# Kernel tuning notes

Hardware: AMD Instinct MI355X
Metric: run time of the kernel (lower is better)

The kernel has to match this reference:

```python
import jax, jax.numpy as jnp
import numpy as np

N = 50000
E = 800000
IN_C = 128
HID = 64
HEADS = 4
EPS = 1e-5
NEG_SLOPE = 0.2


def _glorot(key, shape, fan_in):
    return jax.random.normal(key, shape, dtype=jnp.float32) / np.sqrt(fan_in)


def setup_inputs() -> dict:
    key = jax.random.key(0)
    ks = jax.random.split(key, 32)
    d = {}
    d["x"] = jax.random.normal(ks[0], (N, IN_C), dtype=jnp.float32)
    d["edge_index"] = jax.random.randint(ks[1], (2, E), 0, N, dtype=jnp.int32)
    ph = HID // HEADS  # per-head channels for concat layers (16)
    # Layer 1: in -> [heads, ph], concat
    d["W1"] = _glorot(ks[2], (IN_C, HEADS * ph), IN_C)
    d["a1s"] = _glorot(ks[3], (HEADS, ph), ph)
    d["a1d"] = _glorot(ks[4], (HEADS, ph), ph)
    d["b1"] = jnp.zeros((HID,), jnp.float32)
    # Layer 2: hid -> [heads, ph], concat
    d["W2"] = _glorot(ks[5], (HID, HEADS * ph), HID)
    d["a2s"] = _glorot(ks[6], (HEADS, ph), ph)
    d["a2d"] = _glorot(ks[7], (HEADS, ph), ph)
    d["b2"] = jnp.zeros((HID,), jnp.float32)
    # Layer 3: hid -> [heads, HID], mean over heads (concat=False)
    d["W3"] = _glorot(ks[8], (HID, HEADS * HID), HID)
    d["a3s"] = _glorot(ks[9], (HEADS, HID), HID)
    d["a3d"] = _glorot(ks[10], (HEADS, HID), HID)
    d["b3"] = jnp.zeros((HID,), jnp.float32)
    # BatchNorms (eval mode: running stats)
    for i, k0 in zip((1, 2, 3), (11, 14, 17)):
        d[f"bn{i}_g"] = jnp.ones((HID,), jnp.float32)
        d[f"bn{i}_b"] = jnp.zeros((HID,), jnp.float32)
        d[f"bn{i}_m"] = 0.1 * jax.random.normal(ks[k0], (HID,), dtype=jnp.float32)
        d[f"bn{i}_v"] = jax.random.uniform(ks[k0 + 1], (HID,), minval=0.5, maxval=1.5, dtype=jnp.float32)
    # Classifier MLP: HID -> HID//2 -> 1
    d["cW1"] = _glorot(ks[20], (HID, HID // 2), HID)
    d["cb1"] = jnp.zeros((HID // 2,), jnp.float32)
    d["cW2"] = _glorot(ks[21], (HID // 2, 1), HID // 2)
    d["cb2"] = jnp.zeros((1,), jnp.float32)
    return d


def _gat_layer(x, src, dst, W, a_s, a_d, b, concat):
    n = x.shape[0]
    heads, outc = a_s.shape
    h = (x @ W).reshape(n, heads, outc)           # [N,H,C]
    al_s = jnp.einsum("nhc,hc->nh", h, a_s)       # [N,H]
    al_d = jnp.einsum("nhc,hc->nh", h, a_d)
    e = jax.nn.leaky_relu(al_s[src] + al_d[dst], NEG_SLOPE)  # [E,H]
    m = jax.ops.segment_max(e, dst, num_segments=n)
    ex = jnp.exp(e - m[dst])
    den = jax.ops.segment_sum(ex, dst, num_segments=n)
    alpha = ex / den[dst]                          # segment softmax over dst
    out = jax.ops.segment_sum(h[src] * alpha[..., None], dst, num_segments=n)  # [N,H,C]
    if concat:
        out = out.reshape(n, heads * outc)
    else:
        out = out.mean(axis=1)
    return out + b


def _bn(x, g, b, m, v):
    return g * (x - m) * jax.lax.rsqrt(v + EPS) + b


def reference(x, edge_index, W1, a1s, a1d, b1, W2, a2s, a2d, b2, W3, a3s, a3d, b3,
              bn1_g, bn1_b, bn1_m, bn1_v, bn2_g, bn2_b, bn2_m, bn2_v,
              bn3_g, bn3_b, bn3_m, bn3_v, cW1, cb1, cW2, cb2):
    n = x.shape[0]
    # PyG GATConv adds self-loops by default
    loop = jnp.arange(n, dtype=edge_index.dtype)
    src = jnp.concatenate([edge_index[0], loop])
    dst = jnp.concatenate([edge_index[1], loop])

    h = _gat_layer(x, src, dst, W1, a1s, a1d, b1, concat=True)
    h = jax.nn.elu(_bn(h, bn1_g, bn1_b, bn1_m, bn1_v))
    h = _gat_layer(h, src, dst, W2, a2s, a2d, b2, concat=True)
    h = jax.nn.elu(_bn(h, bn2_g, bn2_b, bn2_m, bn2_v))
    h = _gat_layer(h, src, dst, W3, a3s, a3d, b3, concat=False)
    h = _bn(h, bn3_g, bn3_b, bn3_m, bn3_v)

    h = jax.nn.elu(h @ cW1 + cb1)
    out = (h @ cW2 + cb2).squeeze(-1)  # [N]
    return out
```

## Files before the change

### kernel.cpp

```cpp
#include <hip/hip_runtime.h>

#define HH 4

__device__ __forceinline__ float lrelu(float v){ return v > 0.f ? v : 0.2f*v; }

template<int IC>
__global__ void gemm_gat(const float* __restrict__ X, const float* __restrict__ W,
                         const float* __restrict__ a_s, const float* __restrict__ a_d,
                         float* __restrict__ h, float* __restrict__ als, float* __restrict__ ald,
                         int N) {
    int t = threadIdx.x, lane = t & 63, wid = t >> 6;
    int n = blockIdx.x*4 + wid;
    bool valid = n < N;
    int nc = valid ? n : N-1;
    __shared__ float xs[4][IC];
    #pragma unroll
    for (int k = lane; k < IC; k += 64) xs[wid][k] = X[(size_t)nc*IC + k];
    float acc = 0.f;
    #pragma unroll 8
    for (int k = 0; k < IC; ++k) acc += xs[wid][k] * W[k*64 + lane];
    if (valid) h[(size_t)nc*64 + lane] = acc;
    int hh = lane >> 4, c = lane & 15;
    float ps = acc * a_s[hh*16 + c];
    float pd = acc * a_d[hh*16 + c];
    #pragma unroll
    for (int m = 1; m < 16; m <<= 1){ ps += __shfl_xor(ps, m); pd += __shfl_xor(pd, m); }
    if (valid && c == 0){ als[nc*HH + hh] = ps; ald[nc*HH + hh] = pd; }
}


__global__ void zero_i32(int* __restrict__ p, int n){
    int i = blockIdx.x*256 + threadIdx.x;
    if (i < n) p[i] = 0;
}

__global__ void count_deg(const int* __restrict__ ei, int* __restrict__ deg, int E){
    int e = blockIdx.x*256 + threadIdx.x;
    if (e < E) atomicAdd(&deg[ei[E + e]], 1);
}

__global__ void deg_bsum(const int* __restrict__ deg, int* __restrict__ bsum, int N){
    int t = threadIdx.x;
    int base = blockIdx.x*1024 + t*4;
    int s = 0;
    if (base + 3 < N){
        int4 v = *(const int4*)(deg + base);
        s = v.x + v.y + v.z + v.w;
    } else {
        for (int q = 0; q < 4; ++q) if (base + q < N) s += deg[base + q];
    }
    #pragma unroll
    for (int m = 1; m < 64; m <<= 1) s += __shfl_xor(s, m);
    __shared__ int ws[4];
    if ((t & 63) == 0) ws[t >> 6] = s;
    __syncthreads();
    if (t == 0) bsum[blockIdx.x] = ws[0] + ws[1] + ws[2] + ws[3];
}

__global__ void scan_write(const int* __restrict__ deg, const int* __restrict__ bsum,
                           int* __restrict__ row_off, int* __restrict__ cursor, int N, int E){
    int t = threadIdx.x, bid = blockIdx.x, lane = t & 63, w = t >> 6;
    int base = bid*1024 + t*4;
    int v0 = 0, v1 = 0, v2 = 0, v3 = 0;
    if (base + 3 < N){
        int4 v = *(const int4*)(deg + base);
        v0 = v.x; v1 = v.y; v2 = v.z; v3 = v.w;
    } else {
        if (base     < N) v0 = deg[base];
        if (base + 1 < N) v1 = deg[base + 1];
        if (base + 2 < N) v2 = deg[base + 2];
        if (base + 3 < N) v3 = deg[base + 3];
    }
    int s = v0 + v1 + v2 + v3;
    int x = s;
    #pragma unroll
    for (int d = 1; d < 64; d <<= 1){
        int y = __shfl_up(x, d);
        if (lane >= d) x += y;
    }
    __shared__ int wsum[4];
    __shared__ int boff_s;
    if (lane == 63) wsum[w] = x;
    if (t < 64){
        int o = 0;
        for (int i = t; i < bid; i += 64) o += bsum[i];
        #pragma unroll
        for (int m = 1; m < 64; m <<= 1) o += __shfl_xor(o, m);
        if (t == 0) boff_s = o;
    }
    __syncthreads();
    int woff = 0;
    for (int i = 0; i < w; ++i) woff += wsum[i];
    int o = boff_s + woff + (x - s);
    if (base     < N){ row_off[base]     = o; cursor[base]     = o; o += v0; }
    if (base + 1 < N){ row_off[base + 1] = o; cursor[base + 1] = o; o += v1; }
    if (base + 2 < N){ row_off[base + 2] = o; cursor[base + 2] = o; o += v2; }
    if (base + 3 < N){ row_off[base + 3] = o; cursor[base + 3] = o; o += v3; }
    if (t == 0 && bid == 0) row_off[N] = E;
}

__global__ void fill_csr(const int* __restrict__ ei, int* __restrict__ cursor,
                         int* __restrict__ ssrc, int E){
    int e = blockIdx.x*256 + threadIdx.x;
    if (e < E){
        int d = ei[E + e];
        int p = atomicAdd(&cursor[d], 1);
        ssrc[p] = ei[e];
    }
}

__global__ void prep_l3(const float* __restrict__ W3, const float* __restrict__ a3s,
                        const float* __restrict__ a3d, float* __restrict__ ws3,
                        float* __restrict__ wd3, float* __restrict__ W3p){
    int t = threadIdx.x;
    int hh = t >> 6, k = t & 63;
    float ss = 0.f, sd = 0.f;
    for (int c = 0; c < 64; ++c){
        float w = W3[k*256 + hh*64 + c];
        ss += w * a3s[hh*64 + c];
        sd += w * a3d[hh*64 + c];
        W3p[t*64 + c] = 0.25f * w;
    }
    ws3[t] = ss; wd3[t] = sd;
}

template<bool L3PREP>
__global__ void gat_agg16(const int* __restrict__ row_off, const int* __restrict__ ssrc,
                          const float* __restrict__ als, const float* __restrict__ ald,
                          const float* __restrict__ h, const float* __restrict__ b,
                          const float* __restrict__ g, const float* __restrict__ bb,
                          const float* __restrict__ bm, const float* __restrict__ bv,
                          float* __restrict__ out,
                          const float* __restrict__ ws3, const float* __restrict__ wd3,
                          float* __restrict__ als3, float* __restrict__ ald3, int N){
    int t = threadIdx.x, lane = t & 63, wid = t >> 6;
    int n = blockIdx.x*4 + wid;
    if (n >= N) return;
    __shared__ float wl[4][16][4];
    __shared__ int   sl[4][16];
    int j  = lane & 15;
    int hh = lane >> 4;
    int cb = lane & 15;
    int gq = lane >> 4;
    int hd = cb >> 2;
    float ad_w = ald[n*HH + hh];
    float v_hd = __expf(lrelu(als[n*HH + hd] + ald[n*HH + hd]));
    int beg = row_off[n], end = row_off[n+1];
    float4 acc = make_float4(0.f, 0.f, 0.f, 0.f);
    if (lane < 16){
        float4 hs = *(const float4*)(h + (size_t)n*64 + cb*4);
        acc.x = v_hd*hs.x; acc.y = v_hd*hs.y; acc.z = v_hd*hs.z; acc.w = v_hd*hs.w;
    }
    float denp = 0.f;
    for (int c16 = beg; c16 < end; c16 += 16){
        int e = c16 + j;
        int s = n; float ev = 0.f;
        if (e < end){ s = ssrc[e]; ev = __expf(lrelu(als[s*HH + hh] + ad_w)); }
        denp += ev;
        wl[wid][j][hh] = ev;
        if (hh == 0) sl[wid][j] = s;
        int cnt = min(16, end - c16);
        for (int qb = 0; qb < cnt; qb += 8){
            int eA = qb + gq, eB = qb + 4 + gq;
            int   sA = sl[wid][eA],     sB = sl[wid][eB];
            float wA = wl[wid][eA][hd], wB = wl[wid][eB][hd];
            float4 hA = *(const float4*)(h + (size_t)sA*64 + cb*4);
            float4 hB = *(const float4*)(h + (size_t)sB*64 + cb*4);
            acc.x += wA*hA.x; acc.y += wA*hA.y; acc.z += wA*hA.z; acc.w += wA*hA.w;
            acc.x += wB*hB.x; acc.y += wB*hB.y; acc.z += wB*hB.z; acc.w += wB*hB.w;
        }
    }
    #pragma unroll
    for (int m = 1; m < 16; m <<= 1) denp += __shfl_xor(denp, m);
    float den = __shfl(denp, hd << 4) + v_hd;
    #pragma unroll
    for (int m = 16; m < 64; m <<= 1){
        acc.x += __shfl_xor(acc.x, m); acc.y += __shfl_xor(acc.y, m);
        acc.z += __shfl_xor(acc.z, m); acc.w += __shfl_xor(acc.w, m);
    }
    float4 bb4 = *(const float4*)(b  + cb*4);
    float4 gg4 = *(const float4*)(g  + cb*4);
    float4 be4 = *(const float4*)(bb + cb*4);
    float4 bm4 = *(const float4*)(bm + cb*4);
    float4 bv4 = *(const float4*)(bv + cb*4);
    float4 val;
    val.x = gg4.x*(acc.x/den + bb4.x - bm4.x)*rsqrtf(bv4.x + 1e-5f) + be4.x;
    val.y = gg4.y*(acc.y/den + bb4.y - bm4.y)*rsqrtf(bv4.y + 1e-5f) + be4.y;
    val.z = gg4.z*(acc.z/den + bb4.z - bm4.z)*rsqrtf(bv4.z + 1e-5f) + be4.z;
    val.w = gg4.w*(acc.w/den + bb4.w - bm4.w)*rsqrtf(bv4.w + 1e-5f) + be4.w;
    val.x = val.x > 0.f ? val.x : expm1f(val.x);
    val.y = val.y > 0.f ? val.y : expm1f(val.y);
    val.z = val.z > 0.f ? val.z : expm1f(val.z);
    val.w = val.w > 0.f ? val.w : expm1f(val.w);
    if (lane < 16) *(float4*)(out + (size_t)n*64 + cb*4) = val;
    if (L3PREP){
        float4 w_s = *(const float4*)(ws3 + gq*64 + cb*4);
        float4 w_d = *(const float4*)(wd3 + gq*64 + cb*4);
        float ps = val.x*w_s.x + val.y*w_s.y + val.z*w_s.z + val.w*w_s.w;
        float pd = val.x*w_d.x + val.y*w_d.y + val.z*w_d.z + val.w*w_d.w;
        #pragma unroll
        for (int m = 1; m < 16; m <<= 1){ ps += __shfl_xor(ps, m); pd += __shfl_xor(pd, m); }
        if (cb == 0){ als3[n*HH + gq] = ps; ald3[n*HH + gq] = pd; }
    }
}

__global__ void gat_agg3_fused(const int* __restrict__ row_off, const int* __restrict__ ssrc,
                               const float* __restrict__ als, const float* __restrict__ ald,
                               const float* __restrict__ hin, const float* __restrict__ W3p,
                               const float* __restrict__ b, const float* __restrict__ g,
                               const float* __restrict__ bb, const float* __restrict__ bm,
                               const float* __restrict__ bv, float* __restrict__ out, int N){
    int t = threadIdx.x, lane = t & 63, wid = t >> 6;
    int n0 = blockIdx.x*4;
    int n = min(n0 + wid, N-1);
    __shared__ __align__(16) float4 wlds[4][64];
    __shared__ int slds[4][64];
    __shared__ __align__(16) float ysh[4*256];
    __shared__ float red[4][4][64];
    int cb = lane & 15, gq = lane >> 4;
    float4 adv = *(const float4*)(ald + n*4);
    float4 av  = *(const float4*)(als + n*4);
    float v0 = __expf(lrelu(av.x + adv.x)), v1 = __expf(lrelu(av.y + adv.y));
    float v2 = __expf(lrelu(av.z + adv.z)), v3 = __expf(lrelu(av.w + adv.w));
    int beg = row_off[n], end = row_off[n+1];
    float4 acc0 = make_float4(0,0,0,0), acc1 = acc0, acc2 = acc0, acc3 = acc0;
    if (lane < 16){
        float4 hs = *(const float4*)(hin + (size_t)n*64 + cb*4);
        acc0.x = v0*hs.x; acc0.y = v0*hs.y; acc0.z = v0*hs.z; acc0.w = v0*hs.w;
        acc1.x = v1*hs.x; acc1.y = v1*hs.y; acc1.z = v1*hs.z; acc1.w = v1*hs.w;
        acc2.x = v2*hs.x; acc2.y = v2*hs.y; acc2.z = v2*hs.z; acc2.w = v2*hs.w;
        acc3.x = v3*hs.x; acc3.y = v3*hs.y; acc3.z = v3*hs.z; acc3.w = v3*hs.w;
    }
    float dp0 = 0.f, dp1 = 0.f, dp2 = 0.f, dp3 = 0.f;
    for (int c64 = beg; c64 < end; c64 += 64){
        int e = c64 + lane;
        int s = n; float e0 = 0.f, e1 = 0.f, e2 = 0.f, e3 = 0.f;
        if (e < end){
            s = ssrc[e];
            float4 a = *(const float4*)(als + s*4);
            e0 = __expf(lrelu(a.x + adv.x));
            e1 = __expf(lrelu(a.y + adv.y));
            e2 = __expf(lrelu(a.z + adv.z));
            e3 = __expf(lrelu(a.w + adv.w));
        }
        dp0 += e0; dp1 += e1; dp2 += e2; dp3 += e3;
        wlds[wid][lane] = make_float4(e0, e1, e2, e3);
        slds[wid][lane] = s;
        int cn = min(64, end - c64);
        for (int qb = 0; qb < cn; qb += 8){
            int eA = qb + gq, eB = qb + 4 + gq;
            int sA = slds[wid][eA], sB = slds[wid][eB];
            float4 wA = wlds[wid][eA], wB = wlds[wid][eB];
            float4 hA = *(const float4*)(hin + (size_t)sA*64 + cb*4);
            float4 hB = *(const float4*)(hin + (size_t)sB*64 + cb*4);
            acc0.x += wA.x*hA.x; acc0.y += wA.x*hA.y; acc0.z += wA.x*hA.z; acc0.w += wA.x*hA.w;
            acc1.x += wA.y*hA.x; acc1.y += wA.y*hA.y; acc1.z += wA.y*hA.z; acc1.w += wA.y*hA.w;
            acc2.x += wA.z*hA.x; acc2.y += wA.z*hA.y; acc2.z += wA.z*hA.z; acc2.w += wA.z*hA.w;
            acc3.x += wA.w*hA.x; acc3.y += wA.w*hA.y; acc3.z += wA.w*hA.z; acc3.w += wA.w*hA.w;
            acc0.x += wB.x*hB.x; acc0.y += wB.x*hB.y; acc0.z += wB.x*hB.z; acc0.w += wB.x*hB.w;
            acc1.x += wB.y*hB.x; acc1.y += wB.y*hB.y; acc1.z += wB.y*hB.z; acc1.w += wB.y*hB.w;
            acc2.x += wB.z*hB.x; acc2.y += wB.z*hB.y; acc2.z += wB.z*hB.z; acc2.w += wB.z*hB.w;
            acc3.x += wB.w*hB.x; acc3.y += wB.w*hB.y; acc3.z += wB.w*hB.z; acc3.w += wB.w*hB.w;
        }
    }
    #pragma unroll
    for (int m = 1; m < 64; m <<= 1){
        dp0 += __shfl_xor(dp0, m); dp1 += __shfl_xor(dp1, m);
        dp2 += __shfl_xor(dp2, m); dp3 += __shfl_xor(dp3, m);
    }
    #pragma unroll
    for (int m = 16; m < 64; m <<= 1){
        acc0.x += __shfl_xor(acc0.x, m); acc0.y += __shfl_xor(acc0.y, m);
        acc0.z += __shfl_xor(acc0.z, m); acc0.w += __shfl_xor(acc0.w, m);
        acc1.x += __shfl_xor(acc1.x, m); acc1.y += __shfl_xor(acc1.y, m);
        acc1.z += __shfl_xor(acc1.z, m); acc1.w += __shfl_xor(acc1.w, m);
        acc2.x += __shfl_xor(acc2.x, m); acc2.y += __shfl_xor(acc2.y, m);
        acc2.z += __shfl_xor(acc2.z, m); acc2.w += __shfl_xor(acc2.w, m);
        acc3.x += __shfl_xor(acc3.x, m); acc3.y += __shfl_xor(acc3.y, m);
        acc3.z += __shfl_xor(acc3.z, m); acc3.w += __shfl_xor(acc3.w, m);
    }
    if (lane < 16){
        float r0 = 1.f/(v0 + dp0), r1 = 1.f/(v1 + dp1);
        float r2 = 1.f/(v2 + dp2), r3 = 1.f/(v3 + dp3);
        float4 y0 = make_float4(acc0.x*r0, acc0.y*r0, acc0.z*r0, acc0.w*r0);
        float4 y1 = make_float4(acc1.x*r1, acc1.y*r1, acc1.z*r1, acc1.w*r1);
        float4 y2 = make_float4(acc2.x*r2, acc2.y*r2, acc2.z*r2, acc2.w*r2);
        float4 y3 = make_float4(acc3.x*r3, acc3.y*r3, acc3.z*r3, acc3.w*r3);
        *(float4*)&ysh[wid*256 +   0 + cb*4] = y0;
        *(float4*)&ysh[wid*256 +  64 + cb*4] = y1;
        *(float4*)&ysh[wid*256 + 128 + cb*4] = y2;
        *(float4*)&ysh[wid*256 + 192 + cb*4] = y3;
    }
    __syncthreads();
    float a0 = 0.f, a1 = 0.f, a2 = 0.f, a3 = 0.f;
    int jbase = wid*64;
    #pragma unroll 4
    for (int jj = 0; jj < 64; jj += 4){
        int jb = jbase + jj;
        float4 y0 = *(const float4*)&ysh[0*256 + jb];
        float4 y1 = *(const float4*)&ysh[1*256 + jb];
        float4 y2 = *(const float4*)&ysh[2*256 + jb];
        float4 y3 = *(const float4*)&ysh[3*256 + jb];
        float w0 = W3p[(jb    )*64 + lane];
        float w1 = W3p[(jb + 1)*64 + lane];
        float w2 = W3p[(jb + 2)*64 + lane];
        float w3 = W3p[(jb + 3)*64 + lane];
        a0 += y0.x*w0 + y0.y*w1 + y0.z*w2 + y0.w*w3;
        a1 += y1.x*w0 + y1.y*w1 + y1.z*w2 + y1.w*w3;
        a2 += y2.x*w0 + y2.y*w1 + y2.z*w2 + y2.w*w3;
        a3 += y3.x*w0 + y3.y*w1 + y3.z*w2 + y3.w*w3;
    }
    red[wid][0][lane] = a0;
    red[wid][1][lane] = a1;
    red[wid][2][lane] = a2;
    red[wid][3][lane] = a3;
    __syncthreads();
    int nw = n0 + wid;
    if (nw < N){
        float val = red[0][wid][lane] + red[1][wid][lane] +
                    red[2][wid][lane] + red[3][wid][lane] + b[lane];
        out[(size_t)nw*64 + lane] = g[lane]*(val - bm[lane])*rsqrtf(bv[lane] + 1e-5f) + bb[lane];
    }
}

__global__ void classifier(const float* __restrict__ hin, const float* __restrict__ cW1,
                           const float* __restrict__ cb1, const float* __restrict__ cW2,
                           const float* __restrict__ cb2, float* __restrict__ out, int N){
    __shared__ float w1[64*32];
    __shared__ float b1s[32], w2[32];
    int t = threadIdx.x;
    for (int k = t; k < 64*32; k += 256) w1[k] = cW1[k];
    if (t < 32) { b1s[t] = cb1[t]; w2[t] = cW2[t]; }
    __syncthreads();
    int n = blockIdx.x*256 + t;
    if (n >= N) return;
    float hrow[64];
    #pragma unroll
    for (int k = 0; k < 64; ++k) hrow[k] = hin[(size_t)n*64 + k];
    float acc2 = cb2[0];
    #pragma unroll 4
    for (int j = 0; j < 32; ++j) {
        float a = b1s[j];
        #pragma unroll
        for (int k = 0; k < 64; ++k) a += hrow[k]*w1[k*32 + j];
        float e = a > 0.f ? a : expm1f(a);
        acc2 += e * w2[j];
    }
    out[n] = acc2;
}

extern "C" void kernel_launch(void* const* d_in, const int* in_sizes, int n_in,
                              void* d_out, int out_size, void* d_ws, size_t ws_size,
                              hipStream_t stream) {
    const float* x    = (const float*)d_in[0];
    const int*   ei   = (const int*)  d_in[1];
    const float* W1   = (const float*)d_in[2];
    const float* a1s  = (const float*)d_in[3];
    const float* a1d  = (const float*)d_in[4];
    const float* b1   = (const float*)d_in[5];
    const float* W2   = (const float*)d_in[6];
    const float* a2s  = (const float*)d_in[7];
    const float* a2d  = (const float*)d_in[8];
    const float* b2   = (const float*)d_in[9];
    const float* W3   = (const float*)d_in[10];
    const float* a3s  = (const float*)d_in[11];
    const float* a3d  = (const float*)d_in[12];
    const float* b3   = (const float*)d_in[13];
    const float* bn1g = (const float*)d_in[14];
    const float* bn1b = (const float*)d_in[15];
    const float* bn1m = (const float*)d_in[16];
    const float* bn1v = (const float*)d_in[17];
    const float* bn2g = (const float*)d_in[18];
    const float* bn2b = (const float*)d_in[19];
    const float* bn2m = (const float*)d_in[20];
    const float* bn2v = (const float*)d_in[21];
    const float* bn3g = (const float*)d_in[22];
    const float* bn3b = (const float*)d_in[23];
    const float* bn3m = (const float*)d_in[24];
    const float* bn3v = (const float*)d_in[25];
    const float* cW1  = (const float*)d_in[26];
    const float* cb1  = (const float*)d_in[27];
    const float* cW2  = (const float*)d_in[28];
    const float* cb2  = (const float*)d_in[29];

    const int N = in_sizes[0] / 128;
    const int E = in_sizes[1] / 2;

    float* h    = (float*)d_ws;
    float* hin  = h    + (size_t)N*64;
    float* als  = hin  + (size_t)N*64;
    float* ald  = als  + (size_t)N*4;
    float* als3 = ald  + (size_t)N*4;
    float* ald3 = als3 + (size_t)N*4;
    float* ws3  = ald3 + (size_t)N*4;
    float* wd3  = ws3  + 256;
    float* W3p  = wd3  + 256;
    int* deg     = (int*)(W3p + 16384);
    int* row_off = deg + N;
    int* cursor  = row_off + (N + 1);
    int* ssrc    = cursor + N;
    int* bsum    = ssrc + E;

    const int B = 256;
    int gN  = (N + B-1)/B;
    int gE  = (E + B-1)/B;
    int NB  = (N + 1023)/1024;
    int gN4 = (N + 3)/4;

    zero_i32<<<gN, B, 0, stream>>>(deg, N);
    count_deg<<<gE, B, 0, stream>>>(ei, deg, E);
    deg_bsum<<<NB, B, 0, stream>>>(deg, bsum, N);
    scan_write<<<NB, B, 0, stream>>>(deg, bsum, row_off, cursor, N, E);
    fill_csr<<<gE, B, 0, stream>>>(ei, cursor, ssrc, E);
    prep_l3<<<1, 256, 0, stream>>>(W3, a3s, a3d, ws3, wd3, W3p);

    gemm_gat<128><<<gN4, B, 0, stream>>>(x, W1, a1s, a1d, h, als, ald, N);
    gat_agg16<false><<<gN4, B, 0, stream>>>(row_off, ssrc, als, ald, h, b1,
                                            bn1g, bn1b, bn1m, bn1v, hin,
                                            nullptr, nullptr, nullptr, nullptr, N);

    gemm_gat<64><<<gN4, B, 0, stream>>>(hin, W2, a2s, a2d, h, als, ald, N);
    gat_agg16<true><<<gN4, B, 0, stream>>>(row_off, ssrc, als, ald, h, b2,
                                           bn2g, bn2b, bn2m, bn2v, hin,
                                           ws3, wd3, als3, ald3, N);

    gat_agg3_fused<<<gN4, B, 0, stream>>>(row_off, ssrc, als3, ald3, hin, W3p,
                                          b3, bn3g, bn3b, bn3m, bn3v, h, N);

    classifier<<<gN, B, 0, stream>>>(h, cW1, cb1, cW2, cb2, (float*)d_out, N);
}
```

Baseline: 386.5 us.

## Fuse layer-2 GEMM into layer-1 aggregation and classifier into layer-3 kernel

The layer-1 aggregation kernel now also does the 64x64 layer-2 projection per node and computes its attention logits, so the separate gemm_gat<64> launch is gone. The classifier MLP moves into the end of the layer-3 aggregation kernel, using classifier weights staged in shared memory. This removes two launches and two full node-feature round trips through global memory. The gather loops are also widened to issue four neighbour loads per iteration. The costs are extra shared memory, higher register pressure in the fused kernels and a second node-feature buffer in the workspace.

```diff
diff --git a/kernel.cpp b/kernel.cpp
--- a/kernel.cpp
+++ b/kernel.cpp
@@ -124,15 +124,96 @@
     ws3[t] = ss; wd3[t] = sd;
 }
 
-template<bool L3PREP>
-__global__ void gat_agg16(const int* __restrict__ row_off, const int* __restrict__ ssrc,
-                          const float* __restrict__ als, const float* __restrict__ ald,
-                          const float* __restrict__ h, const float* __restrict__ b,
-                          const float* __restrict__ g, const float* __restrict__ bb,
-                          const float* __restrict__ bm, const float* __restrict__ bv,
-                          float* __restrict__ out,
-                          const float* __restrict__ ws3, const float* __restrict__ wd3,
-                          float* __restrict__ als3, float* __restrict__ ald3, int N){
+__global__ void gat_agg16_l1(const int* __restrict__ row_off, const int* __restrict__ ssrc,
+                             const float* __restrict__ als, const float* __restrict__ ald,
+                             const float* __restrict__ h, const float* __restrict__ b,
+                             const float* __restrict__ g, const float* __restrict__ bb,
+                             const float* __restrict__ bm, const float* __restrict__ bv,
+                             const float* __restrict__ W2, const float* __restrict__ a2s,
+                             const float* __restrict__ a2d, float* __restrict__ h2,
+                             float* __restrict__ als2, float* __restrict__ ald2, int N){
+    int t = threadIdx.x, lane = t & 63, wid = t >> 6;
+    __shared__ float wl[4][16][4];
+    __shared__ int   sl[4][16];
+    __shared__ __align__(16) float vb[4][64];
+    int n = blockIdx.x*4 + wid;
+    if (n >= N) return;
+    int j  = lane & 15;
+    int hh = lane >> 4;
+    int cb = lane & 15;
+    int gq = lane >> 4;
+    int hd = cb >> 2;
+    float ad_w = ald[n*HH + hh];
+    float v_hd = __expf(lrelu(als[n*HH + hd] + ald[n*HH + hd]));
+    int beg = row_off[n], end = row_off[n+1];
+    float4 acc = make_float4(0.f, 0.f, 0.f, 0.f);
+    if (lane < 16){
+        float4 hs = *(const float4*)(h + (size_t)n*64 + cb*4);
+        acc.x = v_hd*hs.x; acc.y = v_hd*hs.y; acc.z = v_hd*hs.z; acc.w = v_hd*hs.w;
+    }
+    float denp = 0.f;
+    for (int c16 = beg; c16 < end; c16 += 16){
+        int e = c16 + j;
+        int s = n; float ev = 0.f;
+        if (e < end){ s = ssrc[e]; ev = __expf(lrelu(als[s*HH + hh] + ad_w)); }
+        denp += ev;
+        wl[wid][j][hh] = ev;
+        if (hh == 0) sl[wid][j] = s;
+        int   s0 = sl[wid][gq],     s1 = sl[wid][4+gq];
+        int   s2 = sl[wid][8+gq],   s3 = sl[wid][12+gq];
+        float w0 = wl[wid][gq][hd], w1 = wl[wid][4+gq][hd];
+        float w2 = wl[wid][8+gq][hd], w3 = wl[wid][12+gq][hd];
+        float4 h0 = *(const float4*)(h + (size_t)s0*64 + cb*4);
+        float4 h1 = *(const float4*)(h + (size_t)s1*64 + cb*4);
+        float4 h2v = *(const float4*)(h + (size_t)s2*64 + cb*4);
+        float4 h3 = *(const float4*)(h + (size_t)s3*64 + cb*4);
+        acc.x += w0*h0.x + w1*h1.x + w2*h2v.x + w3*h3.x;
+        acc.y += w0*h0.y + w1*h1.y + w2*h2v.y + w3*h3.y;
+        acc.z += w0*h0.z + w1*h1.z + w2*h2v.z + w3*h3.z;
+        acc.w += w0*h0.w + w1*h1.w + w2*h2v.w + w3*h3.w;
+    }
+    #pragma unroll
+    for (int m = 1; m < 16; m <<= 1) denp += __shfl_xor(denp, m);
+    float den = __shfl(denp, hd << 4) + v_hd;
+    #pragma unroll
+    for (int m = 16; m < 64; m <<= 1){
+        acc.x += __shfl_xor(acc.x, m); acc.y += __shfl_xor(acc.y, m);
+        acc.z += __shfl_xor(acc.z, m); acc.w += __shfl_xor(acc.w, m);
+    }
+    float4 bb4 = *(const float4*)(b  + cb*4);
+    float4 gg4 = *(const float4*)(g  + cb*4);
+    float4 be4 = *(const float4*)(bb + cb*4);
+    float4 bm4 = *(const float4*)(bm + cb*4);
+    float4 bv4 = *(const float4*)(bv + cb*4);
+    float4 val;
+    val.x = gg4.x*(acc.x/den + bb4.x - bm4.x)*rsqrtf(bv4.x + 1e-5f) + be4.x;
+    val.y = gg4.y*(acc.y/den + bb4.y - bm4.y)*rsqrtf(bv4.y + 1e-5f) + be4.y;
+    val.z = gg4.z*(acc.z/den + bb4.z - bm4.z)*rsqrtf(bv4.z + 1e-5f) + be4.z;
+    val.w = gg4.w*(acc.w/den + bb4.w - bm4.w)*rsqrtf(bv4.w + 1e-5f) + be4.w;
+    val.x = val.x > 0.f ? val.x : expm1f(val.x);
+    val.y = val.y > 0.f ? val.y : expm1f(val.y);
+    val.z = val.z > 0.f ? val.z : expm1f(val.z);
+    val.w = val.w > 0.f ? val.w : expm1f(val.w);
+    if (lane < 16) *(float4*)&vb[wid][cb*4] = val;
+    float acc2 = 0.f;
+    #pragma unroll 8
+    for (int k = 0; k < 64; ++k) acc2 += vb[wid][k] * W2[k*64 + lane];
+    h2[(size_t)n*64 + lane] = acc2;
+    float ps = acc2 * a2s[hh*16 + j];
+    float pd = acc2 * a2d[hh*16 + j];
+    #pragma unroll
+    for (int m = 1; m < 16; m <<= 1){ ps += __shfl_xor(ps, m); pd += __shfl_xor(pd, m); }
+    if (j == 0){ als2[n*HH + hh] = ps; ald2[n*HH + hh] = pd; }
+}
+
+__global__ void gat_agg16_l2(const int* __restrict__ row_off, const int* __restrict__ ssrc,
+                             const float* __restrict__ als, const float* __restrict__ ald,
+                             const float* __restrict__ h, const float* __restrict__ b,
+                             const float* __restrict__ g, const float* __restrict__ bb,
+                             const float* __restrict__ bm, const float* __restrict__ bv,
+                             float* __restrict__ out,
+                             const float* __restrict__ ws3, const float* __restrict__ wd3,
+                             float* __restrict__ als3, float* __restrict__ ald3, int N){
     int t = threadIdx.x, lane = t & 63, wid = t >> 6;
     int n = blockIdx.x*4 + wid;
     if (n >= N) return;
@@ -159,16 +240,18 @@
         denp += ev;
         wl[wid][j][hh] = ev;
         if (hh == 0) sl[wid][j] = s;
-        int cnt = min(16, end - c16);
-        for (int qb = 0; qb < cnt; qb += 8){
-            int eA = qb + gq, eB = qb + 4 + gq;
-            int   sA = sl[wid][eA],     sB = sl[wid][eB];
-            float wA = wl[wid][eA][hd], wB = wl[wid][eB][hd];
-            float4 hA = *(const float4*)(h + (size_t)sA*64 + cb*4);
-            float4 hB = *(const float4*)(h + (size_t)sB*64 + cb*4);
-            acc.x += wA*hA.x; acc.y += wA*hA.y; acc.z += wA*hA.z; acc.w += wA*hA.w;
-            acc.x += wB*hB.x; acc.y += wB*hB.y; acc.z += wB*hB.z; acc.w += wB*hB.w;
-        }
+        int   s0 = sl[wid][gq],     s1 = sl[wid][4+gq];
+        int   s2 = sl[wid][8+gq],   s3 = sl[wid][12+gq];
+        float w0 = wl[wid][gq][hd], w1 = wl[wid][4+gq][hd];
+        float w2 = wl[wid][8+gq][hd], w3 = wl[wid][12+gq][hd];
+        float4 h0 = *(const float4*)(h + (size_t)s0*64 + cb*4);
+        float4 h1 = *(const float4*)(h + (size_t)s1*64 + cb*4);
+        float4 h2v = *(const float4*)(h + (size_t)s2*64 + cb*4);
+        float4 h3 = *(const float4*)(h + (size_t)s3*64 + cb*4);
+        acc.x += w0*h0.x + w1*h1.x + w2*h2v.x + w3*h3.x;
+        acc.y += w0*h0.y + w1*h1.y + w2*h2v.y + w3*h3.y;
+        acc.z += w0*h0.z + w1*h1.z + w2*h2v.z + w3*h3.z;
+        acc.w += w0*h0.w + w1*h1.w + w2*h2v.w + w3*h3.w;
     }
     #pragma unroll
     for (int m = 1; m < 16; m <<= 1) denp += __shfl_xor(denp, m);
@@ -193,15 +276,13 @@
     val.z = val.z > 0.f ? val.z : expm1f(val.z);
     val.w = val.w > 0.f ? val.w : expm1f(val.w);
     if (lane < 16) *(float4*)(out + (size_t)n*64 + cb*4) = val;
-    if (L3PREP){
-        float4 w_s = *(const float4*)(ws3 + gq*64 + cb*4);
-        float4 w_d = *(const float4*)(wd3 + gq*64 + cb*4);
-        float ps = val.x*w_s.x + val.y*w_s.y + val.z*w_s.z + val.w*w_s.w;
-        float pd = val.x*w_d.x + val.y*w_d.y + val.z*w_d.z + val.w*w_d.w;
-        #pragma unroll
-        for (int m = 1; m < 16; m <<= 1){ ps += __shfl_xor(ps, m); pd += __shfl_xor(pd, m); }
-        if (cb == 0){ als3[n*HH + gq] = ps; ald3[n*HH + gq] = pd; }
-    }
+    float4 w_s = *(const float4*)(ws3 + gq*64 + cb*4);
+    float4 w_d = *(const float4*)(wd3 + gq*64 + cb*4);
+    float ps = val.x*w_s.x + val.y*w_s.y + val.z*w_s.z + val.w*w_s.w;
+    float pd = val.x*w_d.x + val.y*w_d.y + val.z*w_d.z + val.w*w_d.w;
+    #pragma unroll
+    for (int m = 1; m < 16; m <<= 1){ ps += __shfl_xor(ps, m); pd += __shfl_xor(pd, m); }
+    if (cb == 0){ als3[n*HH + gq] = ps; ald3[n*HH + gq] = pd; }
 }
 
 __global__ void gat_agg3_fused(const int* __restrict__ row_off, const int* __restrict__ ssrc,
@@ -209,14 +290,23 @@
                                const float* __restrict__ hin, const float* __restrict__ W3p,
                                const float* __restrict__ b, const float* __restrict__ g,
                                const float* __restrict__ bb, const float* __restrict__ bm,
-                               const float* __restrict__ bv, float* __restrict__ out, int N){
+                               const float* __restrict__ bv,
+                               const float* __restrict__ cW1, const float* __restrict__ cb1,
+                               const float* __restrict__ cW2, const float* __restrict__ cb2,
+                               float* __restrict__ dout, int N){
     int t = threadIdx.x, lane = t & 63, wid = t >> 6;
     int n0 = blockIdx.x*4;
     int n = min(n0 + wid, N-1);
+    bool valid = (n0 + wid) < N;
     __shared__ __align__(16) float4 wlds[4][64];
     __shared__ int slds[4][64];
     __shared__ __align__(16) float ysh[4*256];
     __shared__ float red[4][4][64];
+    __shared__ float cls1[64*32];
+    __shared__ float clb[32], clw2[32];
+    __shared__ float ysc[4][64];
+    for (int k = t; k < 2048; k += 256) cls1[k] = cW1[k];
+    if (t < 32){ clb[t] = cb1[t]; clw2[t] = cW2[t]; }
     int cb = lane & 15, gq = lane >> 4;
     float4 adv = *(const float4*)(ald + n*4);
     float4 av  = *(const float4*)(als + n*4);
@@ -247,20 +337,31 @@
         wlds[wid][lane] = make_float4(e0, e1, e2, e3);
         slds[wid][lane] = s;
         int cn = min(64, end - c64);
-        for (int qb = 0; qb < cn; qb += 8){
-            int eA = qb + gq, eB = qb + 4 + gq;
-            int sA = slds[wid][eA], sB = slds[wid][eB];
-            float4 wA = wlds[wid][eA], wB = wlds[wid][eB];
+        for (int qb = 0; qb < cn; qb += 16){
+            int sA = slds[wid][qb + gq],      sB = slds[wid][qb + 4 + gq];
+            int sC = slds[wid][qb + 8 + gq],  sD = slds[wid][qb + 12 + gq];
+            float4 wA = wlds[wid][qb + gq],     wB = wlds[wid][qb + 4 + gq];
+            float4 wC = wlds[wid][qb + 8 + gq], wD = wlds[wid][qb + 12 + gq];
             float4 hA = *(const float4*)(hin + (size_t)sA*64 + cb*4);
             float4 hB = *(const float4*)(hin + (size_t)sB*64 + cb*4);
-            acc0.x += wA.x*hA.x; acc0.y += wA.x*hA.y; acc0.z += wA.x*hA.z; acc0.w += wA.x*hA.w;
-            acc1.x += wA.y*hA.x; acc1.y += wA.y*hA.y; acc1.z += wA.y*hA.z; acc1.w += wA.y*hA.w;
-            acc2.x += wA.z*hA.x; acc2.y += wA.z*hA.y; acc2.z += wA.z*hA.z; acc2.w += wA.z*hA.w;
-            acc3.x += wA.w*hA.x; acc3.y += wA.w*hA.y; acc3.z += wA.w*hA.z; acc3.w += wA.w*hA.w;
-            acc0.x += wB.x*hB.x; acc0.y += wB.x*hB.y; acc0.z += wB.x*hB.z; acc0.w += wB.x*hB.w;
-            acc1.x += wB.y*hB.x; acc1.y += wB.y*hB.y; acc1.z += wB.y*hB.z; acc1.w += wB.y*hB.w;
-            acc2.x += wB.z*hB.x; acc2.y += wB.z*hB.y; acc2.z += wB.z*hB.z; acc2.w += wB.z*hB.w;
-            acc3.x += wB.w*hB.x; acc3.y += wB.w*hB.y; acc3.z += wB.w*hB.z; acc3.w += wB.w*hB.w;
+            float4 hC = *(const float4*)(hin + (size_t)sC*64 + cb*4);
+            float4 hD = *(const float4*)(hin + (size_t)sD*64 + cb*4);
+            acc0.x += wA.x*hA.x + wB.x*hB.x + wC.x*hC.x + wD.x*hD.x;
+            acc0.y += wA.x*hA.y + wB.x*hB.y + wC.x*hC.y + wD.x*hD.y;
+            acc0.z += wA.x*hA.z + wB.x*hB.z + wC.x*hC.z + wD.x*hD.z;
+            acc0.w += wA.x*hA.w + wB.x*hB.w + wC.x*hC.w + wD.x*hD.w;
+            acc1.x += wA.y*hA.x + wB.y*hB.x + wC.y*hC.x + wD.y*hD.x;
+            acc1.y += wA.y*hA.y + wB.y*hB.y + wC.y*hC.y + wD.y*hD.y;
+            acc1.z += wA.y*hA.z + wB.y*hB.z + wC.y*hC.z + wD.y*hD.z;
+            acc1.w += wA.y*hA.w + wB.y*hB.w + wC.y*hC.w + wD.y*hD.w;
+            acc2.x += wA.z*hA.x + wB.z*hB.x + wC.z*hC.x + wD.z*hD.x;
+            acc2.y += wA.z*hA.y + wB.z*hB.y + wC.z*hC.y + wD.z*hD.y;
+            acc2.z += wA.z*hA.z + wB.z*hB.z + wC.z*hC.z + wD.z*hD.z;
+            acc2.w += wA.z*hA.w + wB.z*hB.w + wC.z*hC.w + wD.z*hD.w;
+            acc3.x += wA.w*hA.x + wB.w*hB.x + wC.w*hC.x + wD.w*hD.x;
+            acc3.y += wA.w*hA.y + wB.w*hB.y + wC.w*hC.y + wD.w*hD.y;
+            acc3.z += wA.w*hA.z + wB.w*hB.z + wC.w*hC.z + wD.w*hD.z;
+            acc3.w += wA.w*hA.w + wB.w*hB.w + wC.w*hC.w + wD.w*hD.w;
         }
     }
     #pragma unroll
@@ -282,14 +383,10 @@
     if (lane < 16){
         float r0 = 1.f/(v0 + dp0), r1 = 1.f/(v1 + dp1);
         float r2 = 1.f/(v2 + dp2), r3 = 1.f/(v3 + dp3);
-        float4 y0 = make_float4(acc0.x*r0, acc0.y*r0, acc0.z*r0, acc0.w*r0);
-        float4 y1 = make_float4(acc1.x*r1, acc1.y*r1, acc1.z*r1, acc1.w*r1);
-        float4 y2 = make_float4(acc2.x*r2, acc2.y*r2, acc2.z*r2, acc2.w*r2);
-        float4 y3 = make_float4(acc3.x*r3, acc3.y*r3, acc3.z*r3, acc3.w*r3);
-        *(float4*)&ysh[wid*256 +   0 + cb*4] = y0;
-        *(float4*)&ysh[wid*256 +  64 + cb*4] = y1;
-        *(float4*)&ysh[wid*256 + 128 + cb*4] = y2;
-        *(float4*)&ysh[wid*256 + 192 + cb*4] = y3;
+        *(float4*)&ysh[wid*256 +   0 + cb*4] = make_float4(acc0.x*r0, acc0.y*r0, acc0.z*r0, acc0.w*r0);
+        *(float4*)&ysh[wid*256 +  64 + cb*4] = make_float4(acc1.x*r1, acc1.y*r1, acc1.z*r1, acc1.w*r1);
+        *(float4*)&ysh[wid*256 + 128 + cb*4] = make_float4(acc2.x*r2, acc2.y*r2, acc2.z*r2, acc2.w*r2);
+        *(float4*)&ysh[wid*256 + 192 + cb*4] = make_float4(acc3.x*r3, acc3.y*r3, acc3.z*r3, acc3.w*r3);
     }
     __syncthreads();
     float a0 = 0.f, a1 = 0.f, a2 = 0.f, a3 = 0.f;
@@ -315,38 +412,27 @@
     red[wid][2][lane] = a2;
     red[wid][3][lane] = a3;
     __syncthreads();
-    int nw = n0 + wid;
-    if (nw < N){
-        float val = red[0][wid][lane] + red[1][wid][lane] +
-                    red[2][wid][lane] + red[3][wid][lane] + b[lane];
-        out[(size_t)nw*64 + lane] = g[lane]*(val - bm[lane])*rsqrtf(bv[lane] + 1e-5f) + bb[lane];
-    }
-}
-
-__global__ void classifier(const float* __restrict__ hin, const float* __restrict__ cW1,
-                           const float* __restrict__ cb1, const float* __restrict__ cW2,
-                           const float* __restrict__ cb2, float* __restrict__ out, int N){
-    __shared__ float w1[64*32];
-    __shared__ float b1s[32], w2[32];
-    int t = threadIdx.x;
-    for (int k = t; k < 64*32; k += 256) w1[k] = cW1[k];
-    if (t < 32) { b1s[t] = cb1[t]; w2[t] = cW2[t]; }
-    __syncthreads();
-    int n = blockIdx.x*256 + t;
-    if (n >= N) return;
-    float hrow[64];
-    #pragma unroll
-    for (int k = 0; k < 64; ++k) hrow[k] = hin[(size_t)n*64 + k];
-    float acc2 = cb2[0];
-    #pragma unroll 4
-    for (int j = 0; j < 32; ++j) {
-        float a = b1s[j];
-        #pragma unroll
-        for (int k = 0; k < 64; ++k) a += hrow[k]*w1[k*32 + j];
-        float e = a > 0.f ? a : expm1f(a);
-        acc2 += e * w2[j];
-    }
-    out[n] = acc2;
+    float val = red[0][wid][lane] + red[1][wid][lane] +
+                red[2][wid][lane] + red[3][wid][lane] + b[lane];
+    val = g[lane]*(val - bm[lane])*rsqrtf(bv[lane] + 1e-5f) + bb[lane];
+    ysc[wid][lane] = val;
+    int u = lane >> 1, p = lane & 1;
+    float hsum = 0.f;
+    #pragma unroll 8
+    for (int kk = 0; kk < 32; ++kk){
+        int k = p*32 + kk;
+        hsum += ysc[wid][k] * cls1[k*32 + u];
+    }
+    hsum += __shfl_xor(hsum, 1);
+    float contrib = 0.f;
+    if (p == 0){
+        float hv = clb[u] + hsum;
+        hv = hv > 0.f ? hv : expm1f(hv);
+        contrib = hv * clw2[u];
+    }
+    #pragma unroll
+    for (int m = 2; m < 64; m <<= 1) contrib += __shfl_xor(contrib, m);
+    if (lane == 0 && valid) dout[n0 + wid] = contrib + cb2[0];
 }
 
 extern "C" void kernel_launch(void* const* d_in, const int* in_sizes, int n_in,
@@ -387,10 +473,13 @@
     const int E = in_sizes[1] / 2;
 
     float* h    = (float*)d_ws;
-    float* hin  = h    + (size_t)N*64;
+    float* h2   = h    + (size_t)N*64;
+    float* hin  = h2   + (size_t)N*64;
     float* als  = hin  + (size_t)N*64;
     float* ald  = als  + (size_t)N*4;
-    float* als3 = ald  + (size_t)N*4;
+    float* als2 = ald  + (size_t)N*4;
+    float* ald2 = als2 + (size_t)N*4;
+    float* als3 = ald2 + (size_t)N*4;
     float* ald3 = als3 + (size_t)N*4;
     float* ws3  = ald3 + (size_t)N*4;
     float* wd3  = ws3  + 256;
@@ -415,17 +504,16 @@
     prep_l3<<<1, 256, 0, stream>>>(W3, a3s, a3d, ws3, wd3, W3p);
 
     gemm_gat<128><<<gN4, B, 0, stream>>>(x, W1, a1s, a1d, h, als, ald, N);
-    gat_agg16<false><<<gN4, B, 0, stream>>>(row_off, ssrc, als, ald, h, b1,
-                                            bn1g, bn1b, bn1m, bn1v, hin,
-                                            nullptr, nullptr, nullptr, nullptr, N);
-
-    gemm_gat<64><<<gN4, B, 0, stream>>>(hin, W2, a2s, a2d, h, als, ald, N);
-    gat_agg16<true><<<gN4, B, 0, stream>>>(row_off, ssrc, als, ald, h, b2,
-                                           bn2g, bn2b, bn2m, bn2v, hin,
-                                           ws3, wd3, als3, ald3, N);
+
+    gat_agg16_l1<<<gN4, B, 0, stream>>>(row_off, ssrc, als, ald, h, b1,
+                                        bn1g, bn1b, bn1m, bn1v,
+                                        W2, a2s, a2d, h2, als2, ald2, N);
+
+    gat_agg16_l2<<<gN4, B, 0, stream>>>(row_off, ssrc, als2, ald2, h2, b2,
+                                        bn2g, bn2b, bn2m, bn2v, hin,
+                                        ws3, wd3, als3, ald3, N);
 
     gat_agg3_fused<<<gN4, B, 0, stream>>>(row_off, ssrc, als3, ald3, hin, W3p,
-                                          b3, bn3g, bn3b, bn3m, bn3v, h, N);
-
-    classifier<<<gN, B, 0, stream>>>(h, cW1, cb1, cW2, cb2, (float*)d_out, N);
-}
+                                          b3, bn3g, bn3b, bn3m, bn3v,
+                                          cW1, cb1, cW2, cb2, (float*)d_out, N);
+}
```

Result: no change. 389.4 us (+0.8%).
